# Optimization experiments

Measured on AMD Instinct MI355X. Metric: run time of the kernel, lower is better.

## Reference

```python
import jax, jax.numpy as jnp
import numpy as np

N = 6144      # total nodes
G = 32        # graphs
NPG = 192     # nodes per graph (N = G*NPG)
FIN = 32      # num_node_features
FE = 8        # num_edge_features
H = 64        # layers = [64, 64]
HM = 128      # layers_MLP = [128]
C = 2         # num_classes
K = 8         # opts.knn
E = 49152     # given edges
EPS = 1e-5


def _bn(x, g, b):
    # BatchNorm1d in train mode: biased batch stats
    m = x.mean(0)
    v = x.var(0)
    return (x - m) * jax.lax.rsqrt(v + EPS) * g + b


def setup_inputs() -> dict:
    key = jax.random.key(0)
    ks = jax.random.split(key, 24)

    def w(k, shape):
        return (jax.random.normal(k, shape, jnp.float32)
                * (1.0 / np.sqrt(shape[0])).astype(np.float32))

    x = jax.random.normal(ks[0], (N, FIN), jnp.float32)
    edge_index = jax.random.randint(ks[1], (2, E), 0, N)
    edge_attr = jax.random.normal(ks[2], (E, FE), jnp.float32)
    batch = jnp.arange(N, dtype=jnp.int64 if jax.config.jax_enable_x64 else jnp.int32) // NPG
    return dict(
        x=x, edge_index=edge_index, edge_attr=edge_attr, batch=batch,
        # EdgeFeatsConv layer 1: mlp(Linear(2*FIN+FE,H), ReLU, Linear(H,H)) + root weight
        ef_w1=w(ks[3], (2 * FIN + FE, H)), ef_b1=jnp.zeros((H,), jnp.float32),
        ef_w2=w(ks[4], (H, H)), ef_b2=jnp.zeros((H,), jnp.float32),
        ef_wroot=w(ks[5], (FIN, H)),
        bn1_g=jnp.ones((H,), jnp.float32), bn1_b=jnp.zeros((H,), jnp.float32),
        # EdgeConv layer 2: mlp(Linear(2*H,H), ReLU, Linear(H,H)), aggr=max
        ec_w1=w(ks[6], (2 * H, H)), ec_b1=jnp.zeros((H,), jnp.float32),
        ec_w2=w(ks[7], (H, H)), ec_b2=jnp.zeros((H,), jnp.float32),
        bn2_g=jnp.ones((H,), jnp.float32), bn2_b=jnp.zeros((H,), jnp.float32),
        # model2: Linear(H,HM), BN, ReLU, Linear(HM,C)
        m2_w1=w(ks[8], (H, HM)), m2_b1=jnp.zeros((HM,), jnp.float32),
        m2_bng=jnp.ones((HM,), jnp.float32), m2_bnb=jnp.zeros((HM,), jnp.float32),
        m2_w2=w(ks[9], (HM, C)), m2_b2=jnp.zeros((C,), jnp.float32),
    )


def reference(x, edge_index, edge_attr, batch,
              ef_w1, ef_b1, ef_w2, ef_b2, ef_wroot, bn1_g, bn1_b,
              ec_w1, ec_b1, ec_w2, ec_b2, bn2_g, bn2_b,
              m2_w1, m2_b1, m2_bng, m2_bnb, m2_w2, m2_b2):
    src, dst = edge_index[0], edge_index[1]

    # ---- layer 1: EdgeFeatsConv (edge-conditioned message MLP + root weight, aggr=sum)
    m = jnp.concatenate([x[dst], x[src], edge_attr], axis=1) @ ef_w1 + ef_b1
    m = jax.nn.relu(m) @ ef_w2 + ef_b2
    x1 = jax.ops.segment_sum(m, dst, num_segments=N) + x @ ef_wroot
    x1 = _bn(x1, bn1_g, bn1_b)

    # ---- layer 2: dynamic KNN graph (loop=False) + to_undirected, then EdgeConv (aggr=max)
    sq = jnp.sum(x1 * x1, axis=1)
    d2 = sq[:, None] + sq[None, :] - 2.0 * (x1 @ x1.T)       # [N, N]
    d2 = d2.at[jnp.arange(N), jnp.arange(N)].set(jnp.inf)    # no self loops
    _, nbr = jax.lax.top_k(-d2, K)                           # [N, K] nearest neighbors
    dst0 = jnp.repeat(jnp.arange(N), K)
    src0 = nbr.reshape(-1)
    s = jnp.concatenate([src0, dst0])                        # undirected (dups OK: max aggr)
    d = jnp.concatenate([dst0, src0])

    h = jnp.concatenate([x1[d], x1[s] - x1[d]], axis=1) @ ec_w1 + ec_b1
    h = jax.nn.relu(h) @ ec_w2 + ec_b2
    x2 = jax.ops.segment_max(h, d, num_segments=N)
    x2 = _bn(x2, bn2_g, bn2_b)

    # ---- per-graph all-pairs |g_i - g_z| (row order: for z, for i)
    g = x2.reshape(G, NPG, H)
    diff = jnp.abs(g[:, None, :, :] - g[:, :, None, :]).reshape(-1, H)  # [G*NPG*NPG, H]

    # ---- model2 MLP + log_softmax
    h2 = jax.nn.relu(_bn(diff @ m2_w1 + m2_b1, m2_bng, m2_bnb))
    out = h2 @ m2_w2 + m2_b2
    return jax.nn.log_softmax(out, axis=1)
```

## Files before the change

### kernel.cpp

```cpp
#include <hip/hip_runtime.h>

#define NN 6144
#define GG 32
#define NPGc 192
#define FINc 32
#define FEc 8
#define Hc 64
#define HMc 128
#define Kc 8
#define Ec 49152
#define NKc (NN*Kc)
#define RTOTc (GG*NPGc*NPGc)

typedef float f32x4 __attribute__((ext_vector_type(4)));
typedef short bf16x8 __attribute__((ext_vector_type(8)));
typedef unsigned long long u64;

__device__ __forceinline__ unsigned short f2bf(float f){
  unsigned u = __float_as_uint(f);
  unsigned r = u + 0x7fffu + ((u>>16)&1u);
  return (unsigned short)(r>>16);
}
__device__ __forceinline__ unsigned fenc(float f){
  unsigned u = __float_as_uint(f);
  return (u & 0x80000000u) ? ~u : (u | 0x80000000u);
}
__device__ __forceinline__ float fdec(unsigned e){
  unsigned u = (e & 0x80000000u) ? (e & 0x7fffffffu) : ~e;
  return __uint_as_float(u);
}
__device__ __forceinline__ void bub8(u64* t8, u64 k){
#pragma unroll
  for (int q=0;q<8;q++){ u64 cur=t8[q]; u64 lo=(k<cur)?k:cur; u64 hi=(k<cur)?cur:k; t8[q]=lo; k=hi; }
}

__global__ void k_init(float* dbins, float* stats){
  int idx = blockIdx.x*256 + threadIdx.x;
  if (idx < 64*256) dbins[idx] = 0.f;
  if (idx < 768) stats[idx] = 0.f;
}

__global__ __launch_bounds__(256) void k_root(const float* __restrict__ x, const float* __restrict__ wr, float* __restrict__ x1a){
  __shared__ float Ws[FINc*Hc];
  __shared__ float xr[4][FINc];
  int t = threadIdx.x;
  for (int q=t;q<FINc*Hc;q+=256) Ws[q] = wr[q];
  int rg = t>>6, j = t&63;
  int r = blockIdx.x*4 + rg;
  if (j < FINc) xr[rg][j] = x[r*FINc + j];
  __syncthreads();
  float a0=0.f, a1=0.f;
#pragma unroll
  for (int k=0;k<FINc;k+=2){
    a0 = fmaf(xr[rg][k],   Ws[k*Hc+j],     a0);
    a1 = fmaf(xr[rg][k+1], Ws[(k+1)*Hc+j], a1);
  }
  x1a[r*Hc + j] = a0 + a1;
}

__global__ __launch_bounds__(256) void k_edge1(const float* __restrict__ x, const int* __restrict__ ei, const float* __restrict__ ea,
                        const float* __restrict__ w1, const float* __restrict__ b1,
                        const float* __restrict__ w2, const float* __restrict__ b2, float* __restrict__ x1a){
  __shared__ float W1s[72*Hc];
  __shared__ float W2s[Hc*Hc];
  __shared__ float ins[4][80];
  __shared__ float hid[4][Hc];
  int t = threadIdx.x;
  for (int q=t;q<72*Hc;q+=256) W1s[q] = w1[q];
  for (int q=t;q<Hc*Hc;q+=256) W2s[q] = w2[q];
  int eg = t>>6, j = t&63;
  float b1j = b1[j], b2j = b2[j];
  __syncthreads();
  for (int it=0; it<8; it++){
    int e = blockIdx.x*32 + it*4 + eg;
    int s = ei[e], d = ei[Ec + e];
    ins[eg][j] = (j < FINc) ? x[d*FINc + j] : x[s*FINc + (j - FINc)];
    if (j < FEc) ins[eg][64 + j] = ea[e*FEc + j];
    __syncthreads();
    float a0=b1j, a1=0.f, a2=0.f, a3=0.f;
#pragma unroll
    for (int k=0;k<72;k+=4){
      a0 = fmaf(ins[eg][k],   W1s[k*Hc+j],     a0);
      a1 = fmaf(ins[eg][k+1], W1s[(k+1)*Hc+j], a1);
      a2 = fmaf(ins[eg][k+2], W1s[(k+2)*Hc+j], a2);
      a3 = fmaf(ins[eg][k+3], W1s[(k+3)*Hc+j], a3);
    }
    hid[eg][j] = fmaxf((a0+a1)+(a2+a3), 0.f);
    __syncthreads();
    float c0=b2j, c1=0.f, c2=0.f, c3=0.f;
#pragma unroll
    for (int k=0;k<Hc;k+=4){
      c0 = fmaf(hid[eg][k],   W2s[k*Hc+j],     c0);
      c1 = fmaf(hid[eg][k+1], W2s[(k+1)*Hc+j], c1);
      c2 = fmaf(hid[eg][k+2], W2s[(k+2)*Hc+j], c2);
      c3 = fmaf(hid[eg][k+3], W2s[(k+3)*Hc+j], c3);
    }
    atomicAdd(&x1a[d*Hc + j], (c0+c1)+(c2+c3));
    __syncthreads();
  }
}

__global__ __launch_bounds__(256) void k_bn_stats(const float* __restrict__ src, float* __restrict__ gsum, float* __restrict__ gss){
  int t = threadIdx.x;
  int c = t & 63;
  int r0 = blockIdx.x*64 + (t>>6);
  float s=0.f, ss=0.f;
  for (int it=0; it<16; it++){
    int r = r0 + it*4;
    float v = src[r*Hc + c];
    s += v; ss += v*v;
  }
  __shared__ float S[64], SS[64];
  if (t < 64){ S[t]=0.f; SS[t]=0.f; }
  __syncthreads();
  atomicAdd(&S[c], s); atomicAdd(&SS[c], ss);
  __syncthreads();
  if (t < 64){ atomicAdd(&gsum[t], S[t]); atomicAdd(&gss[t], SS[t]); }
}

__global__ void k_bn_fin(const float* gsum, const float* gss, const float* gam, const float* bet, float* sc, float* sh){
  int c = threadIdx.x;
  float mean = gsum[c] / (float)NN;
  float var  = gss[c] / (float)NN - mean*mean;
  float rs = rsqrtf(var + 1e-5f);
  float s = rs * gam[c];
  sc[c] = s; sh[c] = bet[c] - mean*s;
}

__global__ __launch_bounds__(256) void k_apply_bn1_sq(const float* __restrict__ x1a, const float* __restrict__ sc, const float* __restrict__ sh,
                               float* __restrict__ x1bn, float* __restrict__ sqv){
  int t = threadIdx.x;
  int c = t & 63;
  int r = blockIdx.x*4 + (t>>6);
  float v = x1a[r*Hc + c]*sc[c] + sh[c];
  x1bn[r*Hc + c] = v;
  float s = v*v;
#pragma unroll
  for (int off=1; off<64; off<<=1) s += __shfl_xor(s, off, 64);
  if (c == 0) sqv[r] = s;
}

__global__ __launch_bounds__(128) void k_knn(const float* __restrict__ x1bn, const float* __restrict__ sqv, u64* __restrict__ parts, int CH){
  __shared__ __align__(16) float XJ[64][68];
  __shared__ float sqj[64];
  int t = threadIdx.x;
  int i1 = blockIdx.x*256 + t;
  int i2 = i1 + 128;
  float4 xa[16], xb[16];
#pragma unroll
  for (int q=0;q<16;q++){
    xa[q] = *(const float4*)(x1bn + (size_t)i1*Hc + q*4);
    xb[q] = *(const float4*)(x1bn + (size_t)i2*Hc + q*4);
  }
  float sqi1 = sqv[i1], sqi2 = sqv[i2];
  u64 t8a[8], t8b[8];
#pragma unroll
  for (int q=0;q<8;q++){ t8a[q] = ~0ull; t8b[q] = ~0ull; }
  float thra = __uint_as_float(0x7f800000u);
  float thrb = thra;
  int cpc = NN / CH;
  int nsub = cpc >> 6;
  int jbase0 = blockIdx.y * cpc;
  for (int sub=0; sub<nsub; sub++){
    int jb = jbase0 + sub*64;
    __syncthreads();
    {
      int c = t>>1, hh = t&1;
      const float4* srcp = (const float4*)(x1bn + (size_t)(jb + c)*Hc + hh*32);
#pragma unroll
      for (int q=0;q<8;q++) *(float4*)&XJ[c][hh*32 + q*4] = srcp[q];
      if (t < 64) sqj[t] = sqv[jb + t];
    }
    __syncthreads();
    for (int j=0;j<64;j++){
      float sqjc = sqj[j];
      float a0=0.f,a1=0.f,a2=0.f,a3=0.f,b0=0.f,b1=0.f,b2=0.f,b3=0.f;
#pragma unroll
      for (int q=0;q<16;q++){
        float4 xj = *(const float4*)&XJ[j][q*4];
        a0=fmaf(xa[q].x,xj.x,a0); a1=fmaf(xa[q].y,xj.y,a1); a2=fmaf(xa[q].z,xj.z,a2); a3=fmaf(xa[q].w,xj.w,a3);
        b0=fmaf(xb[q].x,xj.x,b0); b1=fmaf(xb[q].y,xj.y,b1); b2=fmaf(xb[q].z,xj.z,b2); b3=fmaf(xb[q].w,xj.w,b3);
      }
      float dot1 = (a0+a1)+(a2+a3);
      float dot2 = (b0+b1)+(b2+b3);
      int jj = jb + j;
      float d2a = (sqi1 + sqjc) - 2.f*dot1;
      float d2b = (sqi2 + sqjc) - 2.f*dot2;
      bool ia = !(d2a > thra) && (jj != i1);
      bool ib = !(d2b > thrb) && (jj != i2);
      if (__builtin_expect(ia | ib, 0)){
        if (ia){
          u64 ka = (((u64)fenc(d2a))<<32) | (unsigned)jj;
          bub8(t8a, ka);
          thra = fdec((unsigned)(t8a[7]>>32));
        }
        if (ib){
          u64 kb = (((u64)fenc(d2b))<<32) | (unsigned)jj;
          bub8(t8b, kb);
          thrb = fdec((unsigned)(t8b[7]>>32));
        }
      }
    }
  }
  u64* pa = parts + ((size_t)blockIdx.y*NN + i1)*8;
  u64* pb = parts + ((size_t)blockIdx.y*NN + i2)*8;
#pragma unroll
  for (int q=0;q<8;q++){ pa[q] = t8a[q]; pb[q] = t8b[q]; }
}

__global__ __launch_bounds__(256) void k_knn_merge(const u64* __restrict__ parts, int CH, unsigned* __restrict__ nbr){
  int r = blockIdx.x*256 + threadIdx.x;
  u64 t8[8];
#pragma unroll
  for (int q=0;q<8;q++) t8[q] = ~0ull;
  for (int ch=0; ch<CH; ch++){
    const u64* p = parts + ((size_t)ch*NN + r)*8;
    u64 k[8];
#pragma unroll
    for (int q=0;q<8;q++) k[q] = p[q];
#pragma unroll
    for (int q=0;q<8;q++){
      if (k[q] >= t8[7]) break;
      bub8(t8, k[q]);
    }
  }
#pragma unroll
  for (int s=0;s<8;s++) nbr[r*Kc + s] = (unsigned)(t8[s] & 0xffffffffu);
}

__global__ void k_zero_cnt(unsigned* rcnt){
  int idx = blockIdx.x*256 + threadIdx.x;
  if (idx < NN) rcnt[idx] = 0u;
}
__global__ void k_rev_cnt(const unsigned* __restrict__ nbr, unsigned* __restrict__ rcnt){
  int e = blockIdx.x*256 + threadIdx.x;
  atomicAdd(&rcnt[nbr[e]], 1u);
}
__global__ __launch_bounds__(256) void k_scan(const unsigned* __restrict__ rcnt, unsigned* __restrict__ rptr, unsigned* __restrict__ rcur){
  __shared__ unsigned ps[256];
  int t = threadIdx.x;
  unsigned loc[24];
  unsigned s = 0;
#pragma unroll
  for (int q=0;q<24;q++){ loc[q] = s; s += rcnt[t*24+q]; }
  ps[t] = s;
  __syncthreads();
  for (int off=1; off<256; off<<=1){
    unsigned v = (t>=off)? ps[t-off] : 0u;
    __syncthreads();
    ps[t] += v;
    __syncthreads();
  }
  unsigned base = (t==0)? 0u : ps[t-1];
#pragma unroll
  for (int q=0;q<24;q++){ unsigned v = base + loc[q]; rptr[t*24+q]=v; rcur[t*24+q]=v; }
  if (t==255) rptr[NN] = ps[255];
}
__global__ void k_rev_fill(const unsigned* __restrict__ nbr, unsigned* __restrict__ rcur, unsigned* __restrict__ rlist){
  int e = blockIdx.x*256 + threadIdx.x;
  unsigned pos = atomicAdd(&rcur[nbr[e]], 1u);
  rlist[pos] = (unsigned)(e >> 3);
}

__global__ __launch_bounds__(256) void k_pq(const float* __restrict__ x1bn, const float* __restrict__ w1, const float* __restrict__ b1,
                                            float* __restrict__ A2, float* __restrict__ Qm){
  __shared__ float xs[16][64];
  int t = threadIdx.x;
  int j = t & 63, w = t >> 6;
  float wa[64], wb[64];
#pragma unroll
  for (int k=0;k<64;k++){
    float wt  = w1[k*64 + j];
    float wbv = w1[(64+k)*64 + j];
    wa[k] = wt - wbv; wb[k] = wbv;
  }
  float b1j = b1[j];
  int nb = blockIdx.x * 16;
  for (int q=t; q<16*64; q+=256) xs[q>>6][q&63] = x1bn[(size_t)(nb + (q>>6))*64 + (q&63)];
  __syncthreads();
#pragma unroll
  for (int it=0; it<4; it++){
    int nl = it*4 + w;
    float a = b1j, qq = 0.f;
#pragma unroll
    for (int k=0;k<64;k++){
      float xv = xs[nl][k];
      a  = fmaf(xv, wa[k], a);
      qq = fmaf(xv, wb[k], qq);
    }
    int n = nb + nl;
    A2[(size_t)n*64 + j] = a;
    Qm[(size_t)n*64 + j] = qq;
  }
}

__global__ __launch_bounds__(128) void k_edge2max(const float* __restrict__ A2, const float* __restrict__ Qm,
        const unsigned* __restrict__ nbr, const unsigned* __restrict__ rptr, const unsigned* __restrict__ rlist,
        const float* __restrict__ w2, const float* __restrict__ b2, float* __restrict__ x2f){
  __shared__ __align__(16) float W2T[64][68];
  __shared__ __align__(16) float hidT[64][132];
  __shared__ unsigned x2s[17][64];
  __shared__ unsigned rp_s[17];
  __shared__ int wslot[128];
  int t = threadIdx.x;
  int d0 = blockIdx.x * 16;
  for (int q=t; q<64*64; q+=128) W2T[q&63][q>>6] = w2[q];
  for (int q=t; q<17*64; q+=128) ((unsigned*)x2s)[q] = 0x007FFFFFu;
  if (t < 17) rp_s[t] = rptr[d0 + t];
  __syncthreads();
  unsigned rp0 = rp_s[0];
  int total_rev = (int)(rp_s[16] - rp0);
  int eg = t & 15, cg = t >> 4;
  int r0 = eg*8, c0 = cg*8;
  float b2v[8];
#pragma unroll
  for (int cc=0;cc<8;cc++) b2v[cc] = b2[c0+cc];
  int ntile = 1 + ((total_rev + 127) >> 7);
  for (int tile=0; tile<ntile; tile++){
    int d, s, active;
    if (tile == 0){
      d = d0 + (t>>3); s = (int)nbr[(size_t)d*8 + (t&7)]; active = 1; wslot[t] = t>>3;
    } else {
      int idx = (tile-1)*128 + t;
      active = idx < total_rev;
      if (active){
        unsigned pos = rp0 + (unsigned)idx;
        int sl = 0;
#pragma unroll
        for (int m=1; m<16; m++) sl += (pos >= rp_s[m]) ? 1 : 0;
        s = (int)rlist[pos];
        d = d0 + sl;
        wslot[t] = sl;
      } else { d = d0; s = 0; wslot[t] = 16; }
    }
    if (active){
      const float* pa = A2 + (size_t)d*64;
      const float* pq = Qm + (size_t)s*64;
#pragma unroll
      for (int c4=0; c4<16; c4++){
        float4 va = *(const float4*)(pa + c4*4);
        float4 vq = *(const float4*)(pq + c4*4);
        hidT[c4*4+0][t] = fmaxf(va.x+vq.x, 0.f);
        hidT[c4*4+1][t] = fmaxf(va.y+vq.y, 0.f);
        hidT[c4*4+2][t] = fmaxf(va.z+vq.z, 0.f);
        hidT[c4*4+3][t] = fmaxf(va.w+vq.w, 0.f);
      }
    } else {
#pragma unroll
      for (int c4=0; c4<16; c4++){
        hidT[c4*4+0][t] = 0.f; hidT[c4*4+1][t] = 0.f;
        hidT[c4*4+2][t] = 0.f; hidT[c4*4+3][t] = 0.f;
      }
    }
    __syncthreads();
    float acc[8][8];
#pragma unroll
    for (int i=0;i<8;i++)
#pragma unroll
      for (int cc=0;cc<8;cc++) acc[i][cc] = 0.f;
    for (int k=0;k<64;k+=4){
      float4 wv[8];
#pragma unroll
      for (int cc=0;cc<8;cc++) wv[cc] = *(const float4*)&W2T[c0+cc][k];
#pragma unroll
      for (int kk=0;kk<4;kk++){
        float4 h0 = *(const float4*)&hidT[k+kk][r0];
        float4 h1 = *(const float4*)&hidT[k+kk][r0+4];
        float hh[8] = {h0.x,h0.y,h0.z,h0.w,h1.x,h1.y,h1.z,h1.w};
#pragma unroll
        for (int i=0;i<8;i++)
#pragma unroll
          for (int cc=0;cc<8;cc++)
            acc[i][cc] = fmaf(hh[i], ((const float*)&wv[cc])[kk], acc[i][cc]);
      }
    }
    int cur = wslot[r0];
    float mx[8];
#pragma unroll
    for (int cc=0;cc<8;cc++) mx[cc] = acc[0][cc];
    for (int i=1;i<8;i++){
      int sl = wslot[r0+i];
      if (sl != cur){
#pragma unroll
        for (int cc=0;cc<8;cc++) atomicMax(&x2s[cur][c0+cc], fenc(mx[cc] + b2v[cc]));
        cur = sl;
#pragma unroll
        for (int cc=0;cc<8;cc++) mx[cc] = acc[i][cc];
      } else {
#pragma unroll
        for (int cc=0;cc<8;cc++) mx[cc] = fmaxf(mx[cc], acc[i][cc]);
      }
    }
#pragma unroll
    for (int cc=0;cc<8;cc++) atomicMax(&x2s[cur][c0+cc], fenc(mx[cc] + b2v[cc]));
    __syncthreads();
  }
#pragma unroll
  for (int q=0;q<8;q++){
    int idx = t + q*128;
    int sl = idx >> 6, c = idx & 63;
    x2f[(size_t)(d0+sl)*64 + c] = fdec(x2s[sl][c]);
  }
}

__global__ __launch_bounds__(256) void k_apply_bn2f(const float* __restrict__ x2f, const float* __restrict__ sc, const float* __restrict__ sh, float* __restrict__ x2bn){
  int idx = blockIdx.x*256 + threadIdx.x;
  int c = idx & 63;
  x2bn[idx] = x2f[idx]*sc[c] + sh[c];
}

__global__ __launch_bounds__(256,2) void k_d_stats(const float* __restrict__ x2bn, const float* __restrict__ w1, float* __restrict__ dbins){
  __shared__ __align__(16) char sm[24576 + 16384 + 1024];
  unsigned char* A = (unsigned char*)sm;
  unsigned char* W = (unsigned char*)sm + 24576;
  float* Ssum = (float*)(sm + 40960);
  int t = threadIdx.x;
  int gid = blockIdx.x; int g = gid / NPGc; int z = gid - g*NPGc;
  const float* xg = x2bn + (size_t)g*NPGc*Hc;
  const float* xz = xg + z*Hc;
  Ssum[t] = 0.f;
#pragma unroll
  for (int q=0;q<8;q++){
    int task = t + 256*q; int c = task & 127; int c4 = task >> 7;
    ushort4 p;
    p.x = f2bf(w1[(4*c4+0)*HMc + c]);
    p.y = f2bf(w1[(4*c4+1)*HMc + c]);
    p.z = f2bf(w1[(4*c4+2)*HMc + c]);
    p.w = f2bf(w1[(4*c4+3)*HMc + c]);
    *(ushort4*)(W + c*128 + ((c4*8) ^ ((c&7)<<4))) = p;
  }
#pragma unroll
  for (int q=0;q<12;q++){
    int task = t + 256*q; int i = task >> 4; int c = task & 15;
    float4 a = *(const float4*)(xg + i*Hc + c*4);
    float4 b = *(const float4*)(xz + c*4);
    ushort4 p;
    p.x = f2bf(fabsf(a.x-b.x)); p.y = f2bf(fabsf(a.y-b.y));
    p.z = f2bf(fabsf(a.z-b.z)); p.w = f2bf(fabsf(a.w-b.w));
    *(ushort4*)(A + i*128 + ((c*8) ^ ((i&7)<<4))) = p;
  }
  __syncthreads();
  int w = t>>6, l = t&63, lr = l&15, lg = l>>4;
  int sw = (lr&7)<<4;
  f32x4 zero = {0.f,0.f,0.f,0.f};
  f32x4 acc[3][8];
#pragma unroll
  for (int r=0;r<3;r++)
#pragma unroll
    for (int c=0;c<8;c++) acc[r][c] = zero;
#pragma unroll
  for (int kk=0;kk<2;kk++){
    bf16x8 af[3], bfr[8];
#pragma unroll
    for (int r=0;r<3;r++){
      int row = (w*3+r)*16 + lr;
      af[r] = *(const bf16x8*)(A + row*128 + ((lg*16 + 64*kk) ^ sw));
    }
#pragma unroll
    for (int c=0;c<8;c++){
      int col = c*16 + lr;
      bfr[c] = *(const bf16x8*)(W + col*128 + ((lg*16 + 64*kk) ^ sw));
    }
#pragma unroll
    for (int r=0;r<3;r++)
#pragma unroll
      for (int c=0;c<8;c++)
        acc[r][c] = __builtin_amdgcn_mfma_f32_16x16x32_bf16(af[r], bfr[c], acc[r][c], 0,0,0);
  }
#pragma unroll
  for (int c=0;c<8;c++){
    int col = c*16 + lr;
    float s=0.f, ss=0.f;
#pragma unroll
    for (int r=0;r<3;r++)
#pragma unroll
      for (int q=0;q<4;q++){ float v = acc[r][c][q]; s += v; ss = fmaf(v,v,ss); }
    s  += __shfl_xor(s, 16, 64);  ss += __shfl_xor(ss, 16, 64);
    s  += __shfl_xor(s, 32, 64);  ss += __shfl_xor(ss, 32, 64);
    if (lg == 0){
      atomicAdd(&Ssum[col], s);
      atomicAdd(&Ssum[128+col], ss);
    }
  }
  __syncthreads();
  if (t < 128){
    int bin = gid & 63;
    atomicAdd(&dbins[bin*256 + t], Ssum[t]);
    atomicAdd(&dbins[bin*256 + 128 + t], Ssum[128+t]);
  }
}

__global__ void k_d_fin(const float* __restrict__ dbins, const float* gam, const float* bet, float* dsc, float* dsh){
  int c = threadIdx.x;
  float s=0.f, ss=0.f;
#pragma unroll 8
  for (int b=0;b<64;b++){ s += dbins[b*256 + c]; ss += dbins[b*256 + 128 + c]; }
  float mean = s / (float)RTOTc;
  float var  = ss / (float)RTOTc - mean*mean;
  float rs = rsqrtf(var + 1e-5f);
  float k = rs * gam[c];
  dsc[c] = k; dsh[c] = bet[c] - mean*k;
}

__global__ __launch_bounds__(256,2) void k_d_main(const float* __restrict__ x2bn, const float* __restrict__ w1,
                         const float* __restrict__ w2, const float* __restrict__ b2g,
                         const float* __restrict__ dsc, const float* __restrict__ dsh, float* __restrict__ out){
  __shared__ __align__(16) char sm[49152 + 4096 + 1024];
  unsigned char* A   = (unsigned char*)sm;
  unsigned char* W   = (unsigned char*)sm + 24576;
  unsigned char* W2T = (unsigned char*)sm + 49152;
  float* sS = (float*)(sm + 53248);
  int t = threadIdx.x;
  int gid = blockIdx.x; int g = gid / NPGc; int z = gid - g*NPGc;
  const float* xg = x2bn + (size_t)g*NPGc*Hc;
  const float* xz = xg + z*Hc;
  if (t < 128){ sS[t] = dsc[t]; sS[128+t] = dsh[t]; }
  {
    int c = t>>4, kc = t&15;
    ushort4 p0 = make_ushort4(0,0,0,0), p1 = make_ushort4(0,0,0,0);
    if (c < 2){
      p0.x = f2bf(w2[(kc*8+0)*2 + c]); p0.y = f2bf(w2[(kc*8+1)*2 + c]);
      p0.z = f2bf(w2[(kc*8+2)*2 + c]); p0.w = f2bf(w2[(kc*8+3)*2 + c]);
      p1.x = f2bf(w2[(kc*8+4)*2 + c]); p1.y = f2bf(w2[(kc*8+5)*2 + c]);
      p1.z = f2bf(w2[(kc*8+6)*2 + c]); p1.w = f2bf(w2[(kc*8+7)*2 + c]);
    }
    int byte = c*256 + ((kc*16) ^ ((c&7)<<4));
    *(ushort4*)(W2T + byte) = p0;
    *(ushort4*)(W2T + byte + 8) = p1;
  }
#pragma unroll
  for (int q=0;q<8;q++){
    int task = t + 256*q; int c = task & 127; int c4 = task >> 7;
    ushort4 p;
    p.x = f2bf(w1[(4*c4+0)*HMc + c]);
    p.y = f2bf(w1[(4*c4+1)*HMc + c]);
    p.z = f2bf(w1[(4*c4+2)*HMc + c]);
    p.w = f2bf(w1[(4*c4+3)*HMc + c]);
    *(ushort4*)(W + c*128 + ((c4*8) ^ ((c&7)<<4))) = p;
  }
#pragma unroll
  for (int q=0;q<12;q++){
    int task = t + 256*q; int i = task >> 4; int c = task & 15;
    float4 a = *(const float4*)(xg + i*Hc + c*4);
    float4 b = *(const float4*)(xz + c*4);
    ushort4 p;
    p.x = f2bf(fabsf(a.x-b.x)); p.y = f2bf(fabsf(a.y-b.y));
    p.z = f2bf(fabsf(a.z-b.z)); p.w = f2bf(fabsf(a.w-b.w));
    *(ushort4*)(A + i*128 + ((c*8) ^ ((i&7)<<4))) = p;
  }
  __syncthreads();
  int w = t>>6, l = t&63, lr = l&15, lg = l>>4;
  int sw = (lr&7)<<4;
  f32x4 zero = {0.f,0.f,0.f,0.f};
  f32x4 acc[3][8];
#pragma unroll
  for (int r=0;r<3;r++)
#pragma unroll
    for (int c=0;c<8;c++) acc[r][c] = zero;
#pragma unroll
  for (int kk=0;kk<2;kk++){
    bf16x8 af[3], bfr[8];
#pragma unroll
    for (int r=0;r<3;r++){
      int row = (w*3+r)*16 + lr;
      af[r] = *(const bf16x8*)(A + row*128 + ((lg*16 + 64*kk) ^ sw));
    }
#pragma unroll
    for (int c=0;c<8;c++){
      int col = c*16 + lr;
      bfr[c] = *(const bf16x8*)(W + col*128 + ((lg*16 + 64*kk) ^ sw));
    }
#pragma unroll
    for (int r=0;r<3;r++)
#pragma unroll
      for (int c=0;c<8;c++)
        acc[r][c] = __builtin_amdgcn_mfma_f32_16x16x32_bf16(af[r], bfr[c], acc[r][c], 0,0,0);
  }
  __syncthreads();
#pragma unroll
  for (int r=0;r<3;r++){
#pragma unroll
    for (int c=0;c<8;c++){
      int col = c*16 + lr;
      float scl = sS[col], shf = sS[128+col];
#pragma unroll
      for (int q=0;q<4;q++){
        int row = (w*3+r)*16 + lg*4 + q;
        float v = fmaxf(acc[r][c][q]*scl + shf, 0.f);
        *(unsigned short*)(A + row*256 + ((col*2) ^ ((row&7)<<4))) = f2bf(v);
      }
    }
  }
  __syncthreads();
  f32x4 acc2[3];
#pragma unroll
  for (int r=0;r<3;r++) acc2[r] = zero;
#pragma unroll
  for (int kk=0;kk<4;kk++){
    bf16x8 bw = *(const bf16x8*)(W2T + lr*256 + ((lg*16 + 64*kk) ^ sw));
#pragma unroll
    for (int r=0;r<3;r++){
      int row = (w*3+r)*16 + lr;
      bf16x8 ah = *(const bf16x8*)(A + row*256 + ((lg*16 + 64*kk) ^ sw));
      acc2[r] = __builtin_amdgcn_mfma_f32_16x16x32_bf16(ah, bw, acc2[r], 0,0,0);
    }
  }
  float b2a = b2g[0], b2b = b2g[1];
  size_t obase = (size_t)gid * NPGc;
#pragma unroll
  for (int r=0;r<3;r++){
#pragma unroll
    for (int q=0;q<4;q++){
      float o = acc2[r][q];
      float oo = __shfl_xor(o, 1, 64);
      if (lr < 2){
        int row = (w*3+r)*16 + lg*4 + q;
        float self = o + ((lr==0) ? b2a : b2b);
        float oth  = oo + ((lr==0) ? b2b : b2a);
        float mx = fmaxf(self, oth);
        float lse = mx + logf(expf(self-mx) + expf(oth-mx));
        out[(obase + row)*2 + lr] = self - lse;
      }
    }
  }
}

extern "C" void kernel_launch(void* const* d_in, const int* in_sizes, int n_in,
                              void* d_out, int out_size, void* d_ws, size_t ws_size,
                              hipStream_t stream){
  const float* x    = (const float*)d_in[0];
  const int*   ei   = (const int*)d_in[1];
  const float* ea   = (const float*)d_in[2];
  const float* efw1 = (const float*)d_in[4];
  const float* efb1 = (const float*)d_in[5];
  const float* efw2 = (const float*)d_in[6];
  const float* efb2 = (const float*)d_in[7];
  const float* efwr = (const float*)d_in[8];
  const float* bn1g = (const float*)d_in[9];
  const float* bn1b = (const float*)d_in[10];
  const float* ecw1 = (const float*)d_in[11];
  const float* ecb1 = (const float*)d_in[12];
  const float* ecw2 = (const float*)d_in[13];
  const float* ecb2 = (const float*)d_in[14];
  const float* bn2g = (const float*)d_in[15];
  const float* bn2b = (const float*)d_in[16];
  const float* m2w1 = (const float*)d_in[17];
  const float* m2bng = (const float*)d_in[19];
  const float* m2bnb = (const float*)d_in[20];
  const float* m2w2  = (const float*)d_in[21];
  const float* m2b2  = (const float*)d_in[22];

  char* ws = (char*)d_ws;
  float*    x1a   = (float*)(ws + 0);
  float*    x1bn  = (float*)(ws + 1572864);
  float*    x2bn  = (float*)(ws + 3145728);
  float*    x2f   = (float*)(ws + 4718592);
  float*    sqv   = (float*)(ws + 6291456);
  unsigned* nbr   = (unsigned*)(ws + 6316032);
  float*    stats = (float*)(ws + 6512640);
  float*    dbins = (float*)(ws + 6515712);
  u64*      parts = (u64*)(ws + 6581248);
  float*    A2    = (float*)(ws + 0);
  float*    Qm    = (float*)(ws + 3145728);
  unsigned* rcnt  = (unsigned*)(ws + 6581248);
  unsigned* rptr  = rcnt + 6400;
  unsigned* rcur  = rptr + 6400;
  unsigned* rlist = rcur + 6400;
  float *g1sum = stats,     *g1ss = stats+64,  *sc1 = stats+128, *sh1 = stats+192;
  float *g2sum = stats+256, *g2ss = stats+320, *sc2 = stats+384, *sh2 = stats+448;
  float *dsc = stats+512, *dsh = stats+640;
  float* outp = (float*)d_out;

  int CH = 96;
  if (ws_size < 6581248ull + (size_t)NN*96*64) CH = 48;
  if (ws_size < 6581248ull + (size_t)NN*48*64) CH = 24;

  k_init<<<64,256,0,stream>>>(dbins, stats);
  k_root<<<1536,256,0,stream>>>(x, efwr, x1a);
  k_edge1<<<1536,256,0,stream>>>(x, ei, ea, efw1, efb1, efw2, efb2, x1a);
  k_bn_stats<<<96,256,0,stream>>>(x1a, g1sum, g1ss);
  k_bn_fin<<<1,64,0,stream>>>(g1sum, g1ss, bn1g, bn1b, sc1, sh1);
  k_apply_bn1_sq<<<1536,256,0,stream>>>(x1a, sc1, sh1, x1bn, sqv);
  dim3 kg(24, CH);
  k_knn<<<kg,128,0,stream>>>(x1bn, sqv, parts, CH);
  k_knn_merge<<<24,256,0,stream>>>(parts, CH, nbr);
  k_zero_cnt<<<24,256,0,stream>>>(rcnt);
  k_rev_cnt<<<192,256,0,stream>>>(nbr, rcnt);
  k_scan<<<1,256,0,stream>>>(rcnt, rptr, rcur);
  k_rev_fill<<<192,256,0,stream>>>(nbr, rcur, rlist);
  k_pq<<<384,256,0,stream>>>(x1bn, ecw1, ecb1, A2, Qm);
  k_edge2max<<<384,128,0,stream>>>(A2, Qm, nbr, rptr, rlist, ecw2, ecb2, x2f);
  k_bn_stats<<<96,256,0,stream>>>(x2f, g2sum, g2ss);
  k_bn_fin<<<1,64,0,stream>>>(g2sum, g2ss, bn2g, bn2b, sc2, sh2);
  k_apply_bn2f<<<1536,256,0,stream>>>(x2f, sc2, sh2, x2bn);
  k_d_stats<<<6144,256,0,stream>>>(x2bn, m2w1, dbins);
  k_d_fin<<<1,128,0,stream>>>(dbins, m2bng, m2bnb, dsc, dsh);
  k_d_main<<<6144,256,0,stream>>>(x2bn, m2w1, m2w2, m2b2, dsc, dsh, outp);
}
```

Measured before the change: 560.9 us.

## Restructure edge-conv layer 1 as node-projected gather with CSR and linear second layer

Replaces the per-edge two-layer MLP with atomics by precomputing per-node projections of x (P1 for the dst half, P2 for the src half) and per-edge projections of edge attributes. A CSR over destination nodes is then built so each dst node sums ReLU(P1+P2[src]+EAc) and applies the second linear layer once to the sum, plus deg*b2. This removes most per-edge matmul work and the global atomics, at the cost of several extra small launches and extra workspace. The KNN kernel also gets a min-blocks-per-CU launch bound and a regrouped inner loop that loads four LDS vectors at a time.

After: 554.1 us. About the same (-1.2%).

```diff
diff --git a/kernel.cpp b/kernel.cpp
--- a/kernel.cpp
+++ b/kernel.cpp
@@ -58,46 +58,154 @@
   x1a[r*Hc + j] = a0 + a1;
 }
 
-__global__ __launch_bounds__(256) void k_edge1(const float* __restrict__ x, const int* __restrict__ ei, const float* __restrict__ ea,
-                        const float* __restrict__ w1, const float* __restrict__ b1,
-                        const float* __restrict__ w2, const float* __restrict__ b2, float* __restrict__ x1a){
-  __shared__ float W1s[72*Hc];
-  __shared__ float W2s[Hc*Hc];
-  __shared__ float ins[4][80];
-  __shared__ float hid[4][Hc];
-  int t = threadIdx.x;
-  for (int q=t;q<72*Hc;q+=256) W1s[q] = w1[q];
-  for (int q=t;q<Hc*Hc;q+=256) W2s[q] = w2[q];
-  int eg = t>>6, j = t&63;
-  float b1j = b1[j], b2j = b2[j];
-  __syncthreads();
-  for (int it=0; it<8; it++){
-    int e = blockIdx.x*32 + it*4 + eg;
-    int s = ei[e], d = ei[Ec + e];
-    ins[eg][j] = (j < FINc) ? x[d*FINc + j] : x[s*FINc + (j - FINc)];
-    if (j < FEc) ins[eg][64 + j] = ea[e*FEc + j];
+__global__ __launch_bounds__(256) void k_eac(const float* __restrict__ ea, const float* __restrict__ w1, float* __restrict__ EAc){
+  __shared__ float Wc[FEc*Hc];
+  int t = threadIdx.x;
+  for (int q=t; q<FEc*Hc; q+=256) Wc[q] = w1[64*Hc + q];
+  __syncthreads();
+  int idx = blockIdx.x*256 + t;
+  int e = idx >> 4, c4 = (idx & 15)*4;
+  float av[8];
+#pragma unroll
+  for (int q=0;q<8;q++) av[q] = ea[e*FEc + q];
+  float4 o = {0.f,0.f,0.f,0.f};
+#pragma unroll
+  for (int q=0;q<8;q++){
+    o.x = fmaf(av[q], Wc[q*Hc + c4+0], o.x);
+    o.y = fmaf(av[q], Wc[q*Hc + c4+1], o.y);
+    o.z = fmaf(av[q], Wc[q*Hc + c4+2], o.z);
+    o.w = fmaf(av[q], Wc[q*Hc + c4+3], o.w);
+  }
+  *(float4*)(EAc + (size_t)e*Hc + c4) = o;
+}
+
+__global__ __launch_bounds__(256) void k_p12(const float* __restrict__ x, const float* __restrict__ w1, const float* __restrict__ b1,
+                                             float* __restrict__ P1, float* __restrict__ P2){
+  __shared__ float xs[16][32];
+  int t = threadIdx.x;
+  int j = t & 63, w = t >> 6;
+  float wa[32], wb[32];
+#pragma unroll
+  for (int k=0;k<32;k++){
+    wa[k] = w1[k*Hc + j];
+    wb[k] = w1[(32+k)*Hc + j];
+  }
+  float b1j = b1[j];
+  int nb = blockIdx.x * 16;
+  for (int q=t; q<16*32; q+=256) xs[q>>5][q&31] = x[(size_t)(nb + (q>>5))*FINc + (q&31)];
+  __syncthreads();
+#pragma unroll
+  for (int it=0; it<4; it++){
+    int nl = it*4 + w;
+    float a = b1j, b = 0.f;
+#pragma unroll
+    for (int k=0;k<32;k++){
+      float xv = xs[nl][k];
+      a = fmaf(xv, wa[k], a);
+      b = fmaf(xv, wb[k], b);
+    }
+    int n = nb + nl;
+    P1[(size_t)n*Hc + j] = a;
+    P2[(size_t)n*Hc + j] = b;
+  }
+}
+
+__global__ void k_zero_cnt(unsigned* rcnt){
+  int idx = blockIdx.x*256 + threadIdx.x;
+  if (idx < NN) rcnt[idx] = 0u;
+}
+__global__ void k_cnt_dst(const int* __restrict__ ei, unsigned* __restrict__ rcnt){
+  int e = blockIdx.x*256 + threadIdx.x;
+  atomicAdd(&rcnt[ei[Ec + e]], 1u);
+}
+__global__ __launch_bounds__(256) void k_scan(const unsigned* __restrict__ rcnt, unsigned* __restrict__ rptr, unsigned* __restrict__ rcur){
+  __shared__ unsigned ps[256];
+  int t = threadIdx.x;
+  unsigned loc[24];
+  unsigned s = 0;
+#pragma unroll
+  for (int q=0;q<24;q++){ loc[q] = s; s += rcnt[t*24+q]; }
+  ps[t] = s;
+  __syncthreads();
+  for (int off=1; off<256; off<<=1){
+    unsigned v = (t>=off)? ps[t-off] : 0u;
     __syncthreads();
-    float a0=b1j, a1=0.f, a2=0.f, a3=0.f;
-#pragma unroll
-    for (int k=0;k<72;k+=4){
-      a0 = fmaf(ins[eg][k],   W1s[k*Hc+j],     a0);
-      a1 = fmaf(ins[eg][k+1], W1s[(k+1)*Hc+j], a1);
-      a2 = fmaf(ins[eg][k+2], W1s[(k+2)*Hc+j], a2);
-      a3 = fmaf(ins[eg][k+3], W1s[(k+3)*Hc+j], a3);
-    }
-    hid[eg][j] = fmaxf((a0+a1)+(a2+a3), 0.f);
+    ps[t] += v;
     __syncthreads();
-    float c0=b2j, c1=0.f, c2=0.f, c3=0.f;
-#pragma unroll
-    for (int k=0;k<Hc;k+=4){
-      c0 = fmaf(hid[eg][k],   W2s[k*Hc+j],     c0);
-      c1 = fmaf(hid[eg][k+1], W2s[(k+1)*Hc+j], c1);
-      c2 = fmaf(hid[eg][k+2], W2s[(k+2)*Hc+j], c2);
-      c3 = fmaf(hid[eg][k+3], W2s[(k+3)*Hc+j], c3);
-    }
-    atomicAdd(&x1a[d*Hc + j], (c0+c1)+(c2+c3));
-    __syncthreads();
-  }
+  }
+  unsigned base = (t==0)? 0u : ps[t-1];
+#pragma unroll
+  for (int q=0;q<24;q++){ unsigned v = base + loc[q]; rptr[t*24+q]=v; rcur[t*24+q]=v; }
+  if (t==255) rptr[NN] = ps[255];
+}
+__global__ void k_fill_dst(const int* __restrict__ ei, unsigned* __restrict__ rcur, unsigned* __restrict__ rlist){
+  int e = blockIdx.x*256 + threadIdx.x;
+  unsigned pos = atomicAdd(&rcur[ei[Ec + e]], 1u);
+  rlist[pos] = (unsigned)e;
+}
+__global__ void k_rev_cnt(const unsigned* __restrict__ nbr, unsigned* __restrict__ rcnt){
+  int e = blockIdx.x*256 + threadIdx.x;
+  atomicAdd(&rcnt[nbr[e]], 1u);
+}
+__global__ void k_rev_fill(const unsigned* __restrict__ nbr, unsigned* __restrict__ rcur, unsigned* __restrict__ rlist){
+  int e = blockIdx.x*256 + threadIdx.x;
+  unsigned pos = atomicAdd(&rcur[nbr[e]], 1u);
+  rlist[pos] = (unsigned)(e >> 3);
+}
+
+__global__ __launch_bounds__(128) void k_node1(const float* __restrict__ P1, const float* __restrict__ P2, const float* __restrict__ EAc,
+        const int* __restrict__ ei, const unsigned* __restrict__ rptr, const unsigned* __restrict__ rlist,
+        const float* __restrict__ w2, const float* __restrict__ b2, float* __restrict__ x1a){
+  __shared__ __align__(16) float accs[16][68];
+  __shared__ __align__(16) float W2T[64][68];
+  __shared__ unsigned rp_s[17];
+  int t = threadIdx.x;
+  int d0 = blockIdx.x * 16;
+  for (int q=t; q<64*64; q+=128) W2T[q&63][q>>6] = w2[q];
+  if (t < 17) rp_s[t] = rptr[d0 + t];
+  __syncthreads();
+  int slot = t>>3, cg = t&7, c0 = cg*8;
+  int n = d0 + slot;
+  float4 p1a = *(const float4*)(P1 + (size_t)n*Hc + c0);
+  float4 p1b = *(const float4*)(P1 + (size_t)n*Hc + c0 + 4);
+  float acc[8];
+#pragma unroll
+  for (int q=0;q<8;q++) acc[q] = 0.f;
+  unsigned beg = rp_s[slot], end = rp_s[slot+1];
+  for (unsigned pos=beg; pos<end; pos++){
+    unsigned e = rlist[pos];
+    int s = ei[e];
+    float4 qa = *(const float4*)(P2 + (size_t)s*Hc + c0);
+    float4 qb = *(const float4*)(P2 + (size_t)s*Hc + c0 + 4);
+    float4 fa = *(const float4*)(EAc + (size_t)e*Hc + c0);
+    float4 fb = *(const float4*)(EAc + (size_t)e*Hc + c0 + 4);
+    acc[0] += fmaxf(p1a.x + qa.x + fa.x, 0.f);
+    acc[1] += fmaxf(p1a.y + qa.y + fa.y, 0.f);
+    acc[2] += fmaxf(p1a.z + qa.z + fa.z, 0.f);
+    acc[3] += fmaxf(p1a.w + qa.w + fa.w, 0.f);
+    acc[4] += fmaxf(p1b.x + qb.x + fb.x, 0.f);
+    acc[5] += fmaxf(p1b.y + qb.y + fb.y, 0.f);
+    acc[6] += fmaxf(p1b.z + qb.z + fb.z, 0.f);
+    acc[7] += fmaxf(p1b.w + qb.w + fb.w, 0.f);
+  }
+  *(float4*)&accs[slot][c0]   = make_float4(acc[0],acc[1],acc[2],acc[3]);
+  *(float4*)&accs[slot][c0+4] = make_float4(acc[4],acc[5],acc[6],acc[7]);
+  __syncthreads();
+  float out[8];
+#pragma unroll
+  for (int q=0;q<8;q++) out[q] = 0.f;
+  for (int k4=0;k4<16;k4++){
+    float4 hv = *(const float4*)&accs[slot][k4*4];
+#pragma unroll
+    for (int cc=0;cc<8;cc++){
+      float4 wv = *(const float4*)&W2T[c0+cc][k4*4];
+      out[cc] = fmaf(hv.x,wv.x, fmaf(hv.y,wv.y, fmaf(hv.z,wv.z, fmaf(hv.w,wv.w, out[cc]))));
+    }
+  }
+  float deg = (float)(end - beg);
+  float* px = x1a + (size_t)n*Hc + c0;
+#pragma unroll
+  for (int cc=0;cc<8;cc++) px[cc] += out[cc] + deg*b2[c0+cc];
 }
 
 __global__ __launch_bounds__(256) void k_bn_stats(const float* __restrict__ src, float* __restrict__ gsum, float* __restrict__ gss){
@@ -140,7 +248,7 @@
   if (c == 0) sqv[r] = s;
 }
 
-__global__ __launch_bounds__(128) void k_knn(const float* __restrict__ x1bn, const float* __restrict__ sqv, u64* __restrict__ parts, int CH){
+__global__ __launch_bounds__(128,2) void k_knn(const float* __restrict__ x1bn, const float* __restrict__ sqv, u64* __restrict__ parts, int CH){
   __shared__ __align__(16) float XJ[64][68];
   __shared__ float sqj[64];
   int t = threadIdx.x;
@@ -176,10 +284,21 @@
       float sqjc = sqj[j];
       float a0=0.f,a1=0.f,a2=0.f,a3=0.f,b0=0.f,b1=0.f,b2=0.f,b3=0.f;
 #pragma unroll
-      for (int q=0;q<16;q++){
-        float4 xj = *(const float4*)&XJ[j][q*4];
-        a0=fmaf(xa[q].x,xj.x,a0); a1=fmaf(xa[q].y,xj.y,a1); a2=fmaf(xa[q].z,xj.z,a2); a3=fmaf(xa[q].w,xj.w,a3);
-        b0=fmaf(xb[q].x,xj.x,b0); b1=fmaf(xb[q].y,xj.y,b1); b2=fmaf(xb[q].z,xj.z,b2); b3=fmaf(xb[q].w,xj.w,b3);
+      for (int q4=0;q4<4;q4++){
+        float4 xj0 = *(const float4*)&XJ[j][q4*16];
+        float4 xj1 = *(const float4*)&XJ[j][q4*16+4];
+        float4 xj2 = *(const float4*)&XJ[j][q4*16+8];
+        float4 xj3 = *(const float4*)&XJ[j][q4*16+12];
+        float4 A0 = xa[q4*4+0], A1 = xa[q4*4+1], A2v = xa[q4*4+2], A3 = xa[q4*4+3];
+        float4 B0 = xb[q4*4+0], B1 = xb[q4*4+1], B2v = xb[q4*4+2], B3 = xb[q4*4+3];
+        a0=fmaf(A0.x,xj0.x,a0); a1=fmaf(A0.y,xj0.y,a1); a2=fmaf(A0.z,xj0.z,a2); a3=fmaf(A0.w,xj0.w,a3);
+        b0=fmaf(B0.x,xj0.x,b0); b1=fmaf(B0.y,xj0.y,b1); b2=fmaf(B0.z,xj0.z,b2); b3=fmaf(B0.w,xj0.w,b3);
+        a0=fmaf(A1.x,xj1.x,a0); a1=fmaf(A1.y,xj1.y,a1); a2=fmaf(A1.z,xj1.z,a2); a3=fmaf(A1.w,xj1.w,a3);
+        b0=fmaf(B1.x,xj1.x,b0); b1=fmaf(B1.y,xj1.y,b1); b2=fmaf(B1.z,xj1.z,b2); b3=fmaf(B1.w,xj1.w,b3);
+        a0=fmaf(A2v.x,xj2.x,a0); a1=fmaf(A2v.y,xj2.y,a1); a2=fmaf(A2v.z,xj2.z,a2); a3=fmaf(A2v.w,xj2.w,a3);
+        b0=fmaf(B2v.x,xj2.x,b0); b1=fmaf(B2v.y,xj2.y,b1); b2=fmaf(B2v.z,xj2.z,b2); b3=fmaf(B2v.w,xj2.w,b3);
+        a0=fmaf(A3.x,xj3.x,a0); a1=fmaf(A3.y,xj3.y,a1); a2=fmaf(A3.z,xj3.z,a2); a3=fmaf(A3.w,xj3.w,a3);
+        b0=fmaf(B3.x,xj3.x,b0); b1=fmaf(B3.y,xj3.y,b1); b2=fmaf(B3.z,xj3.z,b2); b3=fmaf(B3.w,xj3.w,b3);
       }
       float dot1 = (a0+a1)+(a2+a3);
       float dot2 = (b0+b1)+(b2+b3);
@@ -226,40 +345,6 @@
   }
 #pragma unroll
   for (int s=0;s<8;s++) nbr[r*Kc + s] = (unsigned)(t8[s] & 0xffffffffu);
-}
-
-__global__ void k_zero_cnt(unsigned* rcnt){
-  int idx = blockIdx.x*256 + threadIdx.x;
-  if (idx < NN) rcnt[idx] = 0u;
-}
-__global__ void k_rev_cnt(const unsigned* __restrict__ nbr, unsigned* __restrict__ rcnt){
-  int e = blockIdx.x*256 + threadIdx.x;
-  atomicAdd(&rcnt[nbr[e]], 1u);
-}
-__global__ __launch_bounds__(256) void k_scan(const unsigned* __restrict__ rcnt, unsigned* __restrict__ rptr, unsigned* __restrict__ rcur){
-  __shared__ unsigned ps[256];
-  int t = threadIdx.x;
-  unsigned loc[24];
-  unsigned s = 0;
-#pragma unroll
-  for (int q=0;q<24;q++){ loc[q] = s; s += rcnt[t*24+q]; }
-  ps[t] = s;
-  __syncthreads();
-  for (int off=1; off<256; off<<=1){
-    unsigned v = (t>=off)? ps[t-off] : 0u;
-    __syncthreads();
-    ps[t] += v;
-    __syncthreads();
-  }
-  unsigned base = (t==0)? 0u : ps[t-1];
-#pragma unroll
-  for (int q=0;q<24;q++){ unsigned v = base + loc[q]; rptr[t*24+q]=v; rcur[t*24+q]=v; }
-  if (t==255) rptr[NN] = ps[255];
-}
-__global__ void k_rev_fill(const unsigned* __restrict__ nbr, unsigned* __restrict__ rcur, unsigned* __restrict__ rlist){
-  int e = blockIdx.x*256 + threadIdx.x;
-  unsigned pos = atomicAdd(&rcur[nbr[e]], 1u);
-  rlist[pos] = (unsigned)(e >> 3);
 }
 
 __global__ __launch_bounds__(256) void k_pq(const float* __restrict__ x1bn, const float* __restrict__ w1, const float* __restrict__ b1,
@@ -662,10 +747,13 @@
   u64*      parts = (u64*)(ws + 6581248);
   float*    A2    = (float*)(ws + 0);
   float*    Qm    = (float*)(ws + 3145728);
+  float*    P1    = (float*)(ws + 3145728);
+  float*    P2    = (float*)(ws + 4718592);
   unsigned* rcnt  = (unsigned*)(ws + 6581248);
   unsigned* rptr  = rcnt + 6400;
   unsigned* rcur  = rptr + 6400;
   unsigned* rlist = rcur + 6400;
+  float*    EAc   = (float*)(ws + 6581248 + 4194304);
   float *g1sum = stats,     *g1ss = stats+64,  *sc1 = stats+128, *sh1 = stats+192;
   float *g2sum = stats+256, *g2ss = stats+320, *sc2 = stats+384, *sh2 = stats+448;
   float *dsc = stats+512, *dsh = stats+640;
@@ -677,7 +765,13 @@
 
   k_init<<<64,256,0,stream>>>(dbins, stats);
   k_root<<<1536,256,0,stream>>>(x, efwr, x1a);
-  k_edge1<<<1536,256,0,stream>>>(x, ei, ea, efw1, efb1, efw2, efb2, x1a);
+  k_eac<<<3072,256,0,stream>>>(ea, efw1, EAc);
+  k_zero_cnt<<<24,256,0,stream>>>(rcnt);
+  k_cnt_dst<<<192,256,0,stream>>>(ei, rcnt);
+  k_scan<<<1,256,0,stream>>>(rcnt, rptr, rcur);
+  k_fill_dst<<<192,256,0,stream>>>(ei, rcur, rlist);
+  k_p12<<<384,256,0,stream>>>(x, efw1, efb1, P1, P2);
+  k_node1<<<384,128,0,stream>>>(P1, P2, EAc, ei, rptr, rlist, efw2, efb2, x1a);
   k_bn_stats<<<96,256,0,stream>>>(x1a, g1sum, g1ss);
   k_bn_fin<<<1,64,0,stream>>>(g1sum, g1ss, bn1g, bn1b, sc1, sh1);
   k_apply_bn1_sq<<<1536,256,0,stream>>>(x1a, sc1, sh1, x1bn, sqv);
```
